# Kernel tuning notes

Measured on AMD Instinct MI355X. Metric: run time of the kernel, lower is better.

The kernel has to match this reference:

```python
import jax, jax.numpy as jnp
import numpy as np

B, Din, T, G = 8, 512, 1024, 128
DM, H, L, FF = 512, 8, 2, 2048
MAX_PERIOD = 10000.0


def _ln(x, s, b, eps=1e-5):
    m = x.mean(-1, keepdims=True)
    v = ((x - m) ** 2).mean(-1, keepdims=True)
    return (x - m) * jax.lax.rsqrt(v + eps) * s + b


def _rope(x, pos):
    # x: (B,H,S,Dh), pos: (S,)
    dh = x.shape[-1]
    half = dh // 2
    freqs = 1.0 / (MAX_PERIOD ** (jnp.arange(half, dtype=jnp.float32) / half))
    ang = pos[:, None] * freqs[None, :]              # (S, half)
    cos, sin = jnp.cos(ang), jnp.sin(ang)
    x1, x2 = x[..., :half], x[..., half:]
    return jnp.concatenate([x1 * cos - x2 * sin, x1 * sin + x2 * cos], axis=-1)


def _transformer(x, W_in, b_in, ln1_s, ln1_b, Wq, Wk, Wv, Wo, ls1,
                 ln2_s, ln2_b, W1, b1, W2, b2, ls2, lnf_s, lnf_b, W_out, b_out):
    # x: (B, Din, S) conv layout -> (B, S, DM)
    h = jnp.einsum('bds,de->bse', x, W_in) + b_in
    Bx, S, E = h.shape
    dh = E // H
    pos = jnp.arange(S, dtype=jnp.float32)
    scale = 1.0 / jnp.sqrt(jnp.asarray(dh, h.dtype))
    for l in range(Wq.shape[0]):
        y = _ln(h, ln1_s[l], ln1_b[l])
        q = (y @ Wq[l]).reshape(Bx, S, H, dh).transpose(0, 2, 1, 3)
        k = (y @ Wk[l]).reshape(Bx, S, H, dh).transpose(0, 2, 1, 3)
        v = (y @ Wv[l]).reshape(Bx, S, H, dh).transpose(0, 2, 1, 3)
        q, k = _rope(q, pos), _rope(k, pos)
        att = jax.nn.softmax(jnp.einsum('bhqd,bhkd->bhqk', q, k) * scale, axis=-1)
        o = jnp.einsum('bhqk,bhkd->bhqd', att, v).transpose(0, 2, 1, 3).reshape(Bx, S, E)
        h = h + ls1[l] * (o @ Wo[l])
        y = _ln(h, ln2_s[l], ln2_b[l])
        h = h + ls2[l] * (jax.nn.gelu(y @ W1[l] + b1[l]) @ W2[l] + b2[l])
    h = _ln(h, lnf_s, lnf_b)
    return (h @ W_out + b_out).transpose(0, 2, 1)  # (B, Din, S)


def _forward(features, alignment_matrix, num_segments_per_item, params):
    Bx, D, Tt = features.shape
    Gx = alignment_matrix.shape[1]
    ar_t = jnp.arange(Tt, dtype=jnp.int32)
    ar_g = jnp.arange(Gx, dtype=jnp.int32)
    group_mask = ar_g[None, :] < num_segments_per_item[:, None]          # (B,G)
    group_last = (alignment_matrix * ar_t.astype(features.dtype)).max(axis=2).astype(jnp.int32)  # (B,G)
    valid_last = jnp.where(group_mask, group_last, -1)
    frame_lengths = valid_last.max(axis=1) + 1                            # (B,)
    frame_mask = ar_t[None, :] < frame_lengths[:, None]                   # (B,T)
    last_for_count = jnp.where(group_mask, group_last, Tt + 1)
    num_q_before = jnp.sum(last_for_count[:, :, None] < ar_t[None, None, :], axis=1).astype(jnp.int32)  # (B,T)
    frame_dest = ar_t[None, :] + num_q_before                             # (B,T)
    query_dest = group_last + ar_g[None, :] + 1                           # (B,G)
    # mean-pooled query init
    summed = jnp.einsum('bgt,bdt->bgd', alignment_matrix, features)
    counts = jnp.maximum(alignment_matrix.sum(axis=2), 1.0)
    queries = (summed / counts[..., None]).transpose(0, 2, 1)             # (B,D,G)
    source_seq = jnp.concatenate([features, queries], axis=2)             # (B,D,T+G)
    dest = jnp.concatenate([frame_dest, query_dest], axis=1)              # (B,T+G)
    smask = jnp.concatenate([frame_mask, group_mask], axis=1)
    dest_m = jnp.where(smask, dest, Tt + Gx)
    perm = jnp.argsort(dest_m, axis=1)                                    # (B,T+G)
    interleaved = jnp.take_along_axis(source_seq, perm[:, None, :], axis=2)
    tout = _transformer(interleaved, *params)                             # (B,D,T+G)
    inv_perm = jnp.argsort(perm, axis=1)
    qpos = inv_perm[:, Tt:]                                               # (B,G)
    agg = jnp.take_along_axis(tout, qpos[:, None, :], axis=2)             # (B,D,G)
    return jnp.where(group_mask[:, None, :], agg, 0.0)


def setup_inputs() -> dict:
    key = jax.random.key(0)
    ks = jax.random.split(key, 8)
    rng = np.random.default_rng(0)
    align = np.zeros((B, G, T), np.float32)
    num_seg = np.zeros((B,), np.int32)
    for b in range(B):
        n = int(rng.integers(G // 2, G + 1))
        cuts = np.sort(rng.choice(np.arange(1, T), n - 1, replace=False))
        gid = np.searchsorted(cuts, np.arange(T), side='right')
        align[b, gid, np.arange(T)] = 1.0
        num_seg[b] = n
    s = 0.02
    return {
        'features': jax.random.normal(ks[0], (B, Din, T), jnp.float32),
        'alignment_matrix': jnp.asarray(align),
        'num_segments_per_item': jnp.asarray(num_seg),
        'W_in': jax.random.normal(ks[1], (Din, DM), jnp.float32) * s,
        'b_in': jnp.zeros((DM,), jnp.float32),
        'ln1_s': jnp.ones((L, DM), jnp.float32), 'ln1_b': jnp.zeros((L, DM), jnp.float32),
        'Wq': jax.random.normal(ks[2], (L, DM, DM), jnp.float32) * s,
        'Wk': jax.random.normal(ks[3], (L, DM, DM), jnp.float32) * s,
        'Wv': jax.random.normal(ks[4], (L, DM, DM), jnp.float32) * s,
        'Wo': jax.random.normal(ks[5], (L, DM, DM), jnp.float32) * s,
        'ls1': 0.01 * jnp.ones((L, DM), jnp.float32),
        'ln2_s': jnp.ones((L, DM), jnp.float32), 'ln2_b': jnp.zeros((L, DM), jnp.float32),
        'W1': jax.random.normal(ks[6], (L, DM, FF), jnp.float32) * s,
        'b1': jnp.zeros((L, FF), jnp.float32),
        'W2': jax.random.normal(ks[7], (L, FF, DM), jnp.float32) * s,
        'b2': jnp.zeros((L, DM), jnp.float32),
        'ls2': 0.01 * jnp.ones((L, DM), jnp.float32),
        'lnf_s': jnp.ones((DM,), jnp.float32), 'lnf_b': jnp.zeros((DM,), jnp.float32),
        'W_out': jax.random.normal(jax.random.fold_in(key, 9), (DM, Din), jnp.float32) * s,
        'b_out': jnp.zeros((Din,), jnp.float32),
    }


def reference(features, alignment_matrix, num_segments_per_item, W_in, b_in, ln1_s, ln1_b,
              Wq, Wk, Wv, Wo, ls1, ln2_s, ln2_b, W1, b1, W2, b2, ls2, lnf_s, lnf_b, W_out, b_out):
    params = (W_in, b_in, ln1_s, ln1_b, Wq, Wk, Wv, Wo, ls1,
              ln2_s, ln2_b, W1, b1, W2, b2, ls2, lnf_s, lnf_b, W_out, b_out)
    return _forward(features, alignment_matrix, num_segments_per_item, params)
```

## Files before the change

kernel.cpp:

```cpp
#include <hip/hip_runtime.h>
#include <hip/hip_bf16.h>
#include <math.h>

#define NB   8
#define NT   1024
#define NG   128
#define NS   1152
#define NDIN 512
#define NDM  512
#define NH   8
#define NDH  64
#define NFF  2048
#define NL   2

typedef __attribute__((ext_vector_type(4))) float  floatx4;
typedef __attribute__((ext_vector_type(8))) short  shortx8;

__device__ __forceinline__ float gelu_f(float x) {
    float u = 1.5957691216057308f * (x + 0.044715f * x * x * x);
    return x / (1.0f + __expf(-u));
}

__device__ __forceinline__ void gload_lds16(const void* g, void* l) {
    __builtin_amdgcn_global_load_lds((const __attribute__((address_space(1))) unsigned int*)g,
                                     (__attribute__((address_space(3))) unsigned int*)l, 16, 0, 0);
}

__device__ __forceinline__ short f2bfs(float x) {
    __hip_bfloat16 h = __float2bfloat16(x);
    return *(short*)&h;
}
__device__ __forceinline__ unsigned pack_bf2(float a, float b) {
    __hip_bfloat16 x = __float2bfloat16(a), y = __float2bfloat16(b);
    return ((unsigned)(*(unsigned short*)&y) << 16) | (*(unsigned short*)&x);
}

__global__ __launch_bounds__(256) void ropetab_k(float2* __restrict__ tab)
{
    const int idx = blockIdx.x * 256 + threadIdx.x;
    if (idx >= NS * 32) return;
    const int s = idx >> 5, i = idx & 31;
    const float fr = __expf(-(float)i * 0.28782313662425576f);
    const float ang = (float)s * fr;
    tab[idx] = make_float2(cosf(ang), sinf(ang));
}

__global__ __launch_bounds__(256) void pool_k(const float* __restrict__ align,
        const float* __restrict__ features, int* __restrict__ glast,
        float* __restrict__ queries)
{
    __shared__ float redf[256];
    __shared__ int   redi[256];
    __shared__ float aw[NT];
    const int bg = blockIdx.x;
    const int b = bg >> 7;
    const int tid = threadIdx.x;
    const float* arow = align + (size_t)bg * NT;
    float cnt = 0.f, last = 0.f;
    int tmin = NT;
    for (int t = tid; t < NT; t += 256) {
        float a = arow[t];
        cnt += a;
        last = fmaxf(last, a * (float)t);
        if (a > 0.f) tmin = min(tmin, t);
    }
    redf[tid] = cnt; __syncthreads();
    for (int s = 128; s > 0; s >>= 1) { if (tid < s) redf[tid] += redf[tid + s]; __syncthreads(); }
    float c = redf[0]; __syncthreads();
    redf[tid] = last; __syncthreads();
    for (int s = 128; s > 0; s >>= 1) { if (tid < s) redf[tid] = fmaxf(redf[tid], redf[tid + s]); __syncthreads(); }
    float l = redf[0];
    redi[tid] = tmin; __syncthreads();
    for (int s = 128; s > 0; s >>= 1) { if (tid < s) redi[tid] = min(redi[tid], redi[tid + s]); __syncthreads(); }
    const int t0 = redi[0];
    const int t1 = (int)l;
    if (tid == 0) glast[bg] = t1;
    __syncthreads();
    for (int t = t0 + tid; t <= t1; t += 256) aw[t - t0] = arow[t];
    __syncthreads();
    const float invc = 1.0f / fmaxf(c, 1.0f);
    for (int d = tid; d < NDIN; d += 256) {
        const float* frow = features + ((size_t)b * NDIN + d) * NT;
        float s = 0.f;
        for (int t = t0; t <= t1; ++t) s += aw[t - t0] * frow[t];
        queries[(size_t)bg * NDIN + d] = s * invc;
    }
}

__global__ __launch_bounds__(256) void rank_k(const int* __restrict__ glast,
        const int* __restrict__ nsegp, int* __restrict__ perm, int* __restrict__ qpos)
{
    __shared__ int dm[NS];
    __shared__ int gl[NG];
    const int b = blockIdx.y;
    const int tid = threadIdx.x;
    const int j = blockIdx.x * 256 + tid;
    if (tid < NG) gl[tid] = glast[b * NG + tid];
    const int ns = nsegp[b];
    __syncthreads();
    for (int jj = tid; jj < NS; jj += 256) {
        int d;
        if (jj < NT) {
            int t = jj, nq = 0, flen = 0;
            for (int g = 0; g < ns; ++g) {
                flen = max(flen, gl[g] + 1);
                nq += (gl[g] < t) ? 1 : 0;
            }
            d = (t < flen) ? (t + nq) : NS;
        } else {
            int g = jj - NT;
            d = (g < ns) ? (gl[g] + g + 1) : NS;
        }
        dm[jj] = d;
    }
    __syncthreads();
    if (j < NS) {
        const int my = dm[j];
        int r = 0;
        for (int t = 0; t < NS; ++t) {
            int v2 = dm[t];
            r += (v2 < my || (v2 == my && t < j)) ? 1 : 0;
        }
        perm[b * NS + r] = j;
        if (j >= NT) qpos[b * NG + (j - NT)] = r;
    }
}

__global__ __launch_bounds__(256) void buildx_k(const float* __restrict__ features,
        const float* __restrict__ queries, const int* __restrict__ perm,
        __hip_bfloat16* __restrict__ X)
{
    const int idx = blockIdx.x * 256 + threadIdx.x;
    if (idx >= NB * NS * NDIN) return;
    const int d = idx & (NDIN - 1);
    const int p = (idx >> 9) % NS;
    const int b = idx / (NS * NDIN);
    const int j = perm[b * NS + p];
    float v = (j < NT) ? features[((size_t)b * NDIN + d) * NT + j]
                       : queries[((size_t)(b * NG + (j - NT))) * NDIN + d];
    X[idx] = __float2bfloat16(v);
}

__device__ __forceinline__ void wtile(const float* __restrict__ src,
        __hip_bfloat16* __restrict__ dst, int K, int N, int i, int tid, short tile[32][33])
{
    const int gx = N / 32;
    const int n0 = (i % gx) * 32;
    const int k0 = (i / gx) * 32;
    {
        const int r = tid >> 3, c4 = (tid & 7) * 4;
        float4 v = *(const float4*)&src[(size_t)(k0 + r) * N + n0 + c4];
        tile[c4 + 0][r] = f2bfs(v.x);
        tile[c4 + 1][r] = f2bfs(v.y);
        tile[c4 + 2][r] = f2bfs(v.z);
        tile[c4 + 3][r] = f2bfs(v.w);
    }
    __syncthreads();
    {
        const int r = tid >> 3, c4 = (tid & 7) * 4;
        short* dp = (short*)dst + (size_t)(n0 + r) * K + k0 + c4;
        short4 v;
        v.x = tile[r][c4 + 0]; v.y = tile[r][c4 + 1];
        v.z = tile[r][c4 + 2]; v.w = tile[r][c4 + 3];
        *(short4*)dp = v;
    }
}

__global__ __launch_bounds__(256) void wtransall_k(
        const float* W_in, const float* Wq, const float* Wk, const float* Wv,
        const float* Wo, const float* W1, const float* W2, const float* W_out,
        __hip_bfloat16* w_inT, __hip_bfloat16* wqkvT0, __hip_bfloat16* wqkvT1,
        __hip_bfloat16* woT0, __hip_bfloat16* woT1,
        __hip_bfloat16* w1T0, __hip_bfloat16* w1T1,
        __hip_bfloat16* w2T0, __hip_bfloat16* w2T1, __hip_bfloat16* woutT)
{
    __shared__ short tile[32][33];
    const int tid = threadIdx.x;
    const int i = blockIdx.x;
    const float* src; __hip_bfloat16* dst; int K, N, ti;
    if (i < 256) { src = W_in; dst = w_inT; K = 512; N = 512; ti = i; }
    else if (i < 6400) {
        int r = i - 256;
        const int l = r / 3072; r -= l * 3072;
        const size_t o5 = (size_t)l * 262144, o2 = (size_t)l * 1048576;
        if (r < 256)       { src = Wq + o5; dst = (l ? wqkvT1 : wqkvT0);          K = 512;  N = 512;  ti = r; }
        else if (r < 512)  { src = Wk + o5; dst = (l ? wqkvT1 : wqkvT0) + 262144; K = 512;  N = 512;  ti = r - 256; }
        else if (r < 768)  { src = Wv + o5; dst = (l ? wqkvT1 : wqkvT0) + 524288; K = 512;  N = 512;  ti = r - 512; }
        else if (r < 1024) { src = Wo + o5; dst = (l ? woT1 : woT0);              K = 512;  N = 512;  ti = r - 768; }
        else if (r < 2048) { src = W1 + o2; dst = (l ? w1T1 : w1T0);              K = 512;  N = 2048; ti = r - 1024; }
        else               { src = W2 + o2; dst = (l ? w2T1 : w2T0);              K = 2048; N = 512;  ti = r - 2048; }
    }
    else { src = W_out; dst = woutT; K = 512; N = 512; ti = i - 6400; }
    wtile(src, dst, K, N, ti, tid, tile);
}

template <int EPI, int OUTBF>
__global__ __launch_bounds__(256) void bgemm_k(const __hip_bfloat16* __restrict__ A,
        const __hip_bfloat16* __restrict__ Bt, void* __restrict__ Cout,
        const float* __restrict__ bias, int M, int N, int K)
{
    __shared__ __align__(16) short As[128 * 32];
    __shared__ __align__(16) short Bs[128 * 32];
    const int tid = threadIdx.x;
    const int wave = tid >> 6, lane = tid & 63;
    const int quad = lane >> 4, l16 = lane & 15;
    const int wm = wave >> 1, wn = wave & 1;
    const size_t bm = (size_t)blockIdx.y * 128, bn = (size_t)blockIdx.x * 128;
    const int sw = (l16 >> 1) & 3;

    const short* Ag = (const short*)A;
    const short* Bg = (const short*)Bt;
    const int lrow = lane >> 2;
    const int lchunk = (lane & 3) ^ ((lane >> 3) & 3);

    floatx4 acc[4][4];
#pragma unroll
    for (int i = 0; i < 4; ++i)
#pragma unroll
        for (int j = 0; j < 4; ++j) acc[i][j] = (floatx4){0.f, 0.f, 0.f, 0.f};

    for (int k0 = 0; k0 < K; k0 += 32) {
        __syncthreads();
#pragma unroll
        for (int c = 0; c < 2; ++c) {
            const int r0 = (c * 4 + wave) * 16;
            const int row = r0 + lrow;
            gload_lds16(Ag + (bm + row) * (size_t)K + k0 + lchunk * 8, &As[r0 * 32]);
            gload_lds16(Bg + (bn + row) * (size_t)K + k0 + lchunk * 8, &Bs[r0 * 32]);
        }
        __syncthreads();
        shortx8 af[4], bf[4];
#pragma unroll
        for (int t = 0; t < 4; ++t) {
            af[t] = *(const shortx8*)&As[(wm * 64 + t * 16 + l16) * 32 + ((quad ^ sw) * 8)];
            bf[t] = *(const shortx8*)&Bs[(wn * 64 + t * 16 + l16) * 32 + ((quad ^ sw) * 8)];
        }
#pragma unroll
        for (int mt = 0; mt < 4; ++mt)
#pragma unroll
            for (int nt = 0; nt < 4; ++nt)
                acc[mt][nt] = __builtin_amdgcn_mfma_f32_16x16x32_bf16(af[mt], bf[nt], acc[mt][nt], 0, 0, 0);
    }
    const size_t mbase = bm + wm * 64;
    const size_t nbase = bn + wn * 64;
#pragma unroll
    for (int nt = 0; nt < 4; ++nt) {
        const size_t n = nbase + nt * 16 + l16;
        const float bz = bias ? bias[n] : 0.f;
#pragma unroll
        for (int mt = 0; mt < 4; ++mt) {
#pragma unroll
            for (int r = 0; r < 4; ++r) {
                const size_t m = mbase + mt * 16 + quad * 4 + r;
                const size_t off = m * N + n;
                float e = acc[mt][nt][r] + bz;
                if (EPI == 1) e = gelu_f(e);
                if (OUTBF) ((__hip_bfloat16*)Cout)[off] = __float2bfloat16(e);
                else       ((float*)Cout)[off] = e;
            }
        }
    }
}

__global__ __launch_bounds__(256) void bgemmqkv_k(const __hip_bfloat16* __restrict__ A,
        const __hip_bfloat16* __restrict__ Bt, __hip_bfloat16* __restrict__ qh,
        __hip_bfloat16* __restrict__ kh, __hip_bfloat16* __restrict__ vT,
        const float2* __restrict__ tab)
{
    __shared__ __align__(16) short As[128 * 32];
    __shared__ __align__(16) short Bs[128 * 32];
    const int tid = threadIdx.x;
    const int wave = tid >> 6, lane = tid & 63;
    const int quad = lane >> 4, l16 = lane & 15;
    const int wm = wave >> 1, wn = wave & 1;
    const size_t bm = (size_t)blockIdx.y * 128, bn = (size_t)blockIdx.x * 128;
    const int sw = (l16 >> 1) & 3;
    const int K = 512;

    const short* Ag = (const short*)A;
    const short* Bg = (const short*)Bt;
    const int lrow = lane >> 2;
    const int lchunk = (lane & 3) ^ ((lane >> 3) & 3);

    floatx4 acc[4][4];
#pragma unroll
    for (int i = 0; i < 4; ++i)
#pragma unroll
        for (int j = 0; j < 4; ++j) acc[i][j] = (floatx4){0.f, 0.f, 0.f, 0.f};

    for (int k0 = 0; k0 < K; k0 += 32) {
        __syncthreads();
#pragma unroll
        for (int c = 0; c < 2; ++c) {
            const int r0 = (c * 4 + wave) * 16;
            const int row = r0 + lrow;
            gload_lds16(Ag + (bm + row) * (size_t)K + k0 + lchunk * 8, &As[r0 * 32]);
            gload_lds16(Bg + (bn + row) * (size_t)K + k0 + lchunk * 8, &Bs[r0 * 32]);
        }
        __syncthreads();
        shortx8 af[4], bf[4];
#pragma unroll
        for (int t = 0; t < 4; ++t) {
            af[t] = *(const shortx8*)&As[(wm * 64 + t * 16 + l16) * 32 + ((quad ^ sw) * 8)];
            bf[t] = *(const shortx8*)&Bs[(wn * 64 + t * 16 + l16) * 32 + ((quad ^ sw) * 8)];
        }
#pragma unroll
        for (int mt = 0; mt < 4; ++mt)
#pragma unroll
            for (int nt = 0; nt < 4; ++nt)
                acc[mt][nt] = __builtin_amdgcn_mfma_f32_16x16x32_bf16(af[mt], bf[nt], acc[mt][nt], 0, 0, 0);
    }
    const int bidx = (int)(bm / NS);
    const int sbase = (int)(bm - (size_t)bidx * NS) + wm * 64;
    const int region = (int)(bn >> 9);
    if (region < 2) {
        const float qsc = region ? 1.0f : 0.18033688011112043f;
        short* dst = (short*)(region ? kh : qh);
        const int h = (int)((((int)bn & 511) + wn * 64) >> 6);
        const size_t hb = ((size_t)(bidx * NH + h)) * NS;
#pragma unroll
        for (int nt = 0; nt < 2; ++nt) {
            const int d = nt * 16 + l16;
            const float2* tp = tab + d;
#pragma unroll
            for (int mt = 0; mt < 4; ++mt) {
#pragma unroll
                for (int r = 0; r < 4; ++r) {
                    const int s = sbase + mt * 16 + quad * 4 + r;
                    float x1 = acc[mt][nt][r], x2 = acc[mt][nt + 2][r];
                    float2 cs = tp[s * 32];
                    short* dp = dst + (hb + s) * NDH + d;
                    dp[0]  = f2bfs(qsc * (x1 * cs.x - x2 * cs.y));
                    dp[32] = f2bfs(qsc * (x1 * cs.y + x2 * cs.x));
                }
            }
        }
    } else {
        const int base = (int)(bn - 1024) + wn * 64;
#pragma unroll
        for (int nt = 0; nt < 4; ++nt) {
            const int dfull = base + nt * 16 + l16;
            const int h = dfull >> 6, d = dfull & 63;
            short* vp = (short*)vT + ((size_t)(bidx * NH + h) * NDH + d) * NS;
#pragma unroll
            for (int mt = 0; mt < 4; ++mt)
#pragma unroll
                for (int r = 0; r < 4; ++r) {
                    const int s = sbase + mt * 16 + quad * 4 + r;
                    vp[s] = f2bfs(acc[mt][nt][r]);
                }
        }
    }
}

template <int EPI, int OUTBF>
__global__ __launch_bounds__(256) void bgemm64_k(const __hip_bfloat16* __restrict__ A,
        const __hip_bfloat16* __restrict__ Bt, void* __restrict__ Cout,
        const float* __restrict__ bias, const float* __restrict__ ls,
        const float* __restrict__ res, const int* __restrict__ nsegp, int M, int N, int K)
{
    __shared__ __align__(16) short As[64 * 32];
    __shared__ __align__(16) short Bs[128 * 32];
    const int tid = threadIdx.x;
    const int wave = tid >> 6, lane = tid & 63;
    const int quad = lane >> 4, l16 = lane & 15;
    const int wm = wave >> 1, wn = wave & 1;
    const size_t bm = (size_t)blockIdx.y * 64, bn = (size_t)blockIdx.x * 128;
    const int sw = (l16 >> 1) & 3;

    const short* Ag = (const short*)A;
    const short* Bg = (const short*)Bt;
    const int lrow = lane >> 2;
    const int lchunk = (lane & 3) ^ ((lane >> 3) & 3);

    floatx4 acc[2][4];
#pragma unroll
    for (int i = 0; i < 2; ++i)
#pragma unroll
        for (int j = 0; j < 4; ++j) acc[i][j] = (floatx4){0.f, 0.f, 0.f, 0.f};

    for (int k0 = 0; k0 < K; k0 += 32) {
        __syncthreads();
        {
            const int rA = wave * 16;
            gload_lds16(Ag + (bm + rA + lrow) * (size_t)K + k0 + lchunk * 8, &As[rA * 32]);
            const int rB = wave * 32;
            gload_lds16(Bg + (bn + rB + lrow) * (size_t)K + k0 + lchunk * 8, &Bs[rB * 32]);
            gload_lds16(Bg + (bn + rB + 16 + lrow) * (size_t)K + k0 + lchunk * 8, &Bs[(rB + 16) * 32]);
        }
        __syncthreads();
        shortx8 af[2], bf[4];
#pragma unroll
        for (int t = 0; t < 2; ++t)
            af[t] = *(const shortx8*)&As[(wm * 32 + t * 16 + l16) * 32 + ((quad ^ sw) * 8)];
#pragma unroll
        for (int t = 0; t < 4; ++t)
            bf[t] = *(const shortx8*)&Bs[(wn * 64 + t * 16 + l16) * 32 + ((quad ^ sw) * 8)];
#pragma unroll
        for (int mt = 0; mt < 2; ++mt)
#pragma unroll
            for (int nt = 0; nt < 4; ++nt)
                acc[mt][nt] = __builtin_amdgcn_mfma_f32_16x16x32_bf16(af[mt], bf[nt], acc[mt][nt], 0, 0, 0);
    }
    const size_t mbase = bm + wm * 32;
    const size_t nbase = bn + wn * 64;
#pragma unroll
    for (int nt = 0; nt < 4; ++nt) {
        const size_t n = nbase + nt * 16 + l16;
        const float bz = bias ? bias[n] : 0.f;
        const float lz = (EPI == 2) ? ls[n] : 0.f;
#pragma unroll
        for (int mt = 0; mt < 2; ++mt) {
#pragma unroll
            for (int r = 0; r < 4; ++r) {
                const size_t m = mbase + mt * 16 + quad * 4 + r;
                float e = acc[mt][nt][r] + bz;
                if (EPI == 4) {
                    const int b = (int)(m >> 7), g = (int)(m & 127);
                    float val = (g < nsegp[b]) ? e : 0.0f;
                    ((float*)Cout)[(size_t)b * (NDIN * NG) + n * NG + g] = val;
                } else {
                    const size_t off = m * N + n;
                    if (EPI == 2) e = res[off] + lz * e;
                    if (OUTBF) ((__hip_bfloat16*)Cout)[off] = __float2bfloat16(e);
                    else       ((float*)Cout)[off] = e;
                }
            }
        }
    }
}

__global__ __launch_bounds__(256) void lnw_k(const float* __restrict__ in,
        __hip_bfloat16* __restrict__ out, const float* __restrict__ gam, const float* __restrict__ bet)
{
    const int r = blockIdx.x * 4 + (threadIdx.x >> 6);
    const int t = threadIdx.x & 63;
    const float4* xp = (const float4*)(in + (size_t)r * NDM);
    float4 a = xp[t * 2], b4 = xp[t * 2 + 1];
    float s = a.x + a.y + a.z + a.w + b4.x + b4.y + b4.z + b4.w;
#pragma unroll
    for (int o = 1; o < 64; o <<= 1) s += __shfl_xor(s, o);
    const float mean = s * (1.0f / NDM);
    float dx[8] = {a.x - mean, a.y - mean, a.z - mean, a.w - mean,
                   b4.x - mean, b4.y - mean, b4.z - mean, b4.w - mean};
    float v = 0.f;
#pragma unroll
    for (int i = 0; i < 8; ++i) v += dx[i] * dx[i];
#pragma unroll
    for (int o = 1; o < 64; o <<= 1) v += __shfl_xor(v, o);
    const float inv = rsqrtf(v * (1.0f / NDM) + 1e-5f);
    const float4* gp = (const float4*)gam;
    const float4* bp = (const float4*)bet;
    float4 g0 = gp[t * 2], g1 = gp[t * 2 + 1], q0 = bp[t * 2], q1 = bp[t * 2 + 1];
    shortx8 o8;
    o8[0] = f2bfs(dx[0] * inv * g0.x + q0.x);
    o8[1] = f2bfs(dx[1] * inv * g0.y + q0.y);
    o8[2] = f2bfs(dx[2] * inv * g0.z + q0.z);
    o8[3] = f2bfs(dx[3] * inv * g0.w + q0.w);
    o8[4] = f2bfs(dx[4] * inv * g1.x + q1.x);
    o8[5] = f2bfs(dx[5] * inv * g1.y + q1.y);
    o8[6] = f2bfs(dx[6] * inv * g1.z + q1.z);
    o8[7] = f2bfs(dx[7] * inv * g1.w + q1.w);
    *(shortx8*)((short*)out + (size_t)r * NDM + t * 8) = o8;
}

__global__ __launch_bounds__(64) void lnwg_k(const float* __restrict__ h,
        __hip_bfloat16* __restrict__ out, const float* __restrict__ gam, const float* __restrict__ bet,
        const int* __restrict__ qpos)
{
    const int r = blockIdx.x, t = threadIdx.x;
    const int b = r >> 7;
    const int src = qpos[r];
    const float4* xp = (const float4*)(h + ((size_t)(b * NS + src)) * NDM);
    float4 a = xp[t * 2], b4 = xp[t * 2 + 1];
    float s = a.x + a.y + a.z + a.w + b4.x + b4.y + b4.z + b4.w;
#pragma unroll
    for (int o = 1; o < 64; o <<= 1) s += __shfl_xor(s, o);
    const float mean = s * (1.0f / NDM);
    float dx[8] = {a.x - mean, a.y - mean, a.z - mean, a.w - mean,
                   b4.x - mean, b4.y - mean, b4.z - mean, b4.w - mean};
    float v = 0.f;
#pragma unroll
    for (int i = 0; i < 8; ++i) v += dx[i] * dx[i];
#pragma unroll
    for (int o = 1; o < 64; o <<= 1) v += __shfl_xor(v, o);
    const float inv = rsqrtf(v * (1.0f / NDM) + 1e-5f);
    const float4* gp = (const float4*)gam;
    const float4* bp = (const float4*)bet;
    float4 g0 = gp[t * 2], g1 = gp[t * 2 + 1], q0 = bp[t * 2], q1 = bp[t * 2 + 1];
    shortx8 o8;
    o8[0] = f2bfs(dx[0] * inv * g0.x + q0.x);
    o8[1] = f2bfs(dx[1] * inv * g0.y + q0.y);
    o8[2] = f2bfs(dx[2] * inv * g0.z + q0.z);
    o8[3] = f2bfs(dx[3] * inv * g0.w + q0.w);
    o8[4] = f2bfs(dx[4] * inv * g1.x + q1.x);
    o8[5] = f2bfs(dx[5] * inv * g1.y + q1.y);
    o8[6] = f2bfs(dx[6] * inv * g1.z + q1.z);
    o8[7] = f2bfs(dx[7] * inv * g1.w + q1.w);
    *(shortx8*)((short*)out + (size_t)r * NDM + t * 8) = o8;
}

#define FKT 64
#define FKP 68
#define NTL (NS / FKT)
__global__ __launch_bounds__(256) void fattn_k(const __hip_bfloat16* __restrict__ qb,
        const __hip_bfloat16* __restrict__ kb, const __hip_bfloat16* __restrict__ vbT,
        __hip_bfloat16* __restrict__ o)
{
    __shared__ __align__(16) short Ks[FKT * FKP];
    __shared__ __align__(16) short Vt[NDH * FKP];
    __shared__ __align__(16) short Pl[64 * FKP];
    const int tid = threadIdx.x;
    const int wave = tid >> 6, lane = tid & 63;
    const int quad = lane >> 4, l16 = lane & 15;
    const int L = blockIdx.x;
    const int xcd = L & 7, sl = L >> 3;
    const int bh = (xcd << 3) | (sl & 7);
    const int q0 = (sl >> 3) * 64;
    const int bb = bh >> 3, hh = bh & 7;
    const short* qbase = (const short*)qb + (size_t)bh * NS * NDH;
    const short* kbase = (const short*)kb + (size_t)bh * NS * NDH;
    const short* vbase = (const short*)vbT + (size_t)bh * NDH * NS;

    shortx8 Qf0, Qf1;
    {
        const short* qp = qbase + (size_t)(q0 + wave * 16 + l16) * NDH + quad * 8;
        Qf0 = *(const shortx8*)qp;
        Qf1 = *(const shortx8*)(qp + 32);
    }
    floatx4 Oacc[4];
#pragma unroll
    for (int i = 0; i < 4; ++i) Oacc[i] = (floatx4){0.f, 0.f, 0.f, 0.f};
    float l_s = 0.f;

    const int sr = tid >> 2, sc = (tid & 3) * 16;
    const int prow = wave * 16 + l16;
    const short* kg = kbase + (size_t)sr * NDH + sc;
    const short* vg = vbase + (size_t)sr * NS + sc;
    shortx8 pk0 = *(const shortx8*)kg, pk1 = *(const shortx8*)(kg + 8);
    shortx8 pv0 = *(const shortx8*)vg, pv1 = *(const shortx8*)(vg + 8);

    for (int t = 0; t < NTL; ++t) {
        __syncthreads();
        *(shortx8*)&Ks[sr * FKP + sc]     = pk0;
        *(shortx8*)&Ks[sr * FKP + sc + 8] = pk1;
        *(shortx8*)&Vt[sr * FKP + sc]     = pv0;
        *(shortx8*)&Vt[sr * FKP + sc + 8] = pv1;
        __syncthreads();
        if (t + 1 < NTL) {
            kg += FKT * NDH; vg += FKT;
            pk0 = *(const shortx8*)kg; pk1 = *(const shortx8*)(kg + 8);
            pv0 = *(const shortx8*)vg; pv1 = *(const shortx8*)(vg + 8);
        }

        floatx4 S[4];
#pragma unroll
        for (int kbk = 0; kbk < 4; ++kbk) {
            shortx8 kf0 = *(const shortx8*)&Ks[(kbk * 16 + l16) * FKP + quad * 8];
            shortx8 kf1 = *(const shortx8*)&Ks[(kbk * 16 + l16) * FKP + 32 + quad * 8];
            floatx4 sa = (floatx4){0.f, 0.f, 0.f, 0.f};
            sa = __builtin_amdgcn_mfma_f32_16x16x32_bf16(kf0, Qf0, sa, 0, 0, 0);
            sa = __builtin_amdgcn_mfma_f32_16x16x32_bf16(kf1, Qf1, sa, 0, 0, 0);
            S[kbk] = sa;
        }
        float e[16];
        float rs = 0.f;
#pragma unroll
        for (int kbk = 0; kbk < 4; ++kbk)
#pragma unroll
            for (int i = 0; i < 4; ++i) {
                float ee = exp2f(S[kbk][i]);
                e[kbk * 4 + i] = ee;
                rs += ee;
            }
        rs += __shfl_xor(rs, 16);
        rs += __shfl_xor(rs, 32);
        l_s += rs;
#pragma unroll
        for (int kbk = 0; kbk < 4; ++kbk) {
            uint2 u;
            u.x = pack_bf2(e[kbk * 4 + 0], e[kbk * 4 + 1]);
            u.y = pack_bf2(e[kbk * 4 + 2], e[kbk * 4 + 3]);
            *(uint2*)&Pl[prow * FKP + kbk * 16 + quad * 4] = u;
        }
        __asm__ __volatile__("" ::: "memory");
        shortx8 Pf0 = *(const shortx8*)&Pl[prow * FKP + quad * 8];
        shortx8 Pf1 = *(const shortx8*)&Pl[prow * FKP + 32 + quad * 8];
#pragma unroll
        for (int ct = 0; ct < 4; ++ct) {
            shortx8 vf0 = *(const shortx8*)&Vt[(ct * 16 + l16) * FKP + quad * 8];
            shortx8 vf1 = *(const shortx8*)&Vt[(ct * 16 + l16) * FKP + 32 + quad * 8];
            Oacc[ct] = __builtin_amdgcn_mfma_f32_16x16x32_bf16(Pf0, vf0, Oacc[ct], 0, 0, 0);
            Oacc[ct] = __builtin_amdgcn_mfma_f32_16x16x32_bf16(Pf1, vf1, Oacc[ct], 0, 0, 0);
        }
    }
    float lr[4];
#pragma unroll
    for (int i = 0; i < 4; ++i) lr[i] = __shfl(l_s, quad * 4 + i);
#pragma unroll
    for (int i = 0; i < 4; ++i) {
        const float inv = 1.0f / lr[i];
        const int row = q0 + wave * 16 + quad * 4 + i;
        __hip_bfloat16* op = o + ((size_t)(bb * NS + row)) * NDM + hh * NDH + l16;
        op[0]  = __float2bfloat16(Oacc[0][i] * inv);
        op[16] = __float2bfloat16(Oacc[1][i] * inv);
        op[32] = __float2bfloat16(Oacc[2][i] * inv);
        op[48] = __float2bfloat16(Oacc[3][i] * inv);
    }
}

extern "C" void kernel_launch(void* const* d_in, const int* in_sizes, int n_in,
                              void* d_out, int out_size, void* d_ws, size_t ws_size,
                              hipStream_t stream) {
    const float* features = (const float*)d_in[0];
    const float* align    = (const float*)d_in[1];
    const int*   nseg     = (const int*)d_in[2];
    const float* W_in  = (const float*)d_in[3];
    const float* b_in  = (const float*)d_in[4];
    const float* ln1_s = (const float*)d_in[5];
    const float* ln1_b = (const float*)d_in[6];
    const float* Wq = (const float*)d_in[7];
    const float* Wk = (const float*)d_in[8];
    const float* Wv = (const float*)d_in[9];
    const float* Wo = (const float*)d_in[10];
    const float* ls1   = (const float*)d_in[11];
    const float* ln2_s = (const float*)d_in[12];
    const float* ln2_b = (const float*)d_in[13];
    const float* W1 = (const float*)d_in[14];
    const float* b1 = (const float*)d_in[15];
    const float* W2 = (const float*)d_in[16];
    const float* b2 = (const float*)d_in[17];
    const float* ls2   = (const float*)d_in[18];
    const float* lnf_s = (const float*)d_in[19];
    const float* lnf_b = (const float*)d_in[20];
    const float* W_out = (const float*)d_in[21];
    const float* b_out = (const float*)d_in[22];

    const size_t SZ_BSD = (size_t)NB * NS * NDM;

    float* p = (float*)d_ws;
    __hip_bfloat16* w_inT  = (__hip_bfloat16*)p;
    __hip_bfloat16* wqkvT0 = w_inT + 512 * 512;
    __hip_bfloat16* wqkvT1 = wqkvT0 + 1536 * 512;
    __hip_bfloat16* woT0   = wqkvT1 + 1536 * 512;
    __hip_bfloat16* woT1   = woT0 + 512 * 512;
    __hip_bfloat16* w1T0   = woT1 + 512 * 512;
    __hip_bfloat16* w1T1   = w1T0 + 2048 * 512;
    __hip_bfloat16* w2T0   = w1T1 + 2048 * 512;
    __hip_bfloat16* w2T1   = w2T0 + 512 * 2048;
    __hip_bfloat16* woutT  = w2T1 + 512 * 2048;
    int* glast = (int*)(woutT + 512 * 512);
    int* perm  = glast + NB * NG;
    int* qpos  = perm + NB * NS;
    float2* ropetab = (float2*)(qpos + NB * NG);
    p = (float*)(ropetab + NS * 32);

    float* hbuf = p; p += SZ_BSD;
    __hip_bfloat16* ybuf = (__hip_bfloat16*)p;  p += SZ_BSD / 2;
    __hip_bfloat16* obuf = (__hip_bfloat16*)p;  p += SZ_BSD / 2;
    __hip_bfloat16* ubuf = (__hip_bfloat16*)p;  p += SZ_BSD * 2;
    __hip_bfloat16* xin  = (__hip_bfloat16*)p;  p += SZ_BSD / 2;
    float* quer = p; p += (size_t)NB * NG * NDIN;
    __hip_bfloat16* hq = (__hip_bfloat16*)p; p += (size_t)NB * NG * NDM / 2;
    const size_t needed = (size_t)((char*)p - (char*)d_ws);
    if (ws_size < needed) return;

    __hip_bfloat16* qh = ubuf;
    __hip_bfloat16* kh = ubuf + SZ_BSD;
    __hip_bfloat16* vT = xin;

    ropetab_k<<<(NS * 32 + 255) / 256, 256, 0, stream>>>(ropetab);
    wtransall_k<<<6656, 256, 0, stream>>>(W_in, Wq, Wk, Wv, Wo, W1, W2, W_out,
            w_inT, wqkvT0, wqkvT1, woT0, woT1, w1T0, w1T1, w2T0, w2T1, woutT);
    pool_k<<<NB * NG, 256, 0, stream>>>(align, features, glast, quer);
    rank_k<<<dim3((NS + 255) / 256, NB), 256, 0, stream>>>(glast, nseg, perm, qpos);
    buildx_k<<<(NB * NS * NDIN + 255) / 256, 256, 0, stream>>>(features, quer, perm, xin);

    const int M = NB * NS;
    bgemm64_k<0, 0><<<dim3(NDM / 128, M / 64), 256, 0, stream>>>(xin, w_inT, hbuf, b_in, nullptr, nullptr, nullptr, M, NDM, NDIN);

    for (int l = 0; l < NL; ++l) {
        __hip_bfloat16* wqkvT = (l ? wqkvT1 : wqkvT0);
        __hip_bfloat16* woT   = (l ? woT1 : woT0);
        __hip_bfloat16* w1T   = (l ? w1T1 : w1T0);
        __hip_bfloat16* w2T   = (l ? w2T1 : w2T0);

        lnw_k<<<M / 4, 256, 0, stream>>>(hbuf, ybuf, ln1_s + l * NDM, ln1_b + l * NDM);
        bgemmqkv_k<<<dim3(1536 / 128, M / 128), 256, 0, stream>>>(ybuf, wqkvT, qh, kh, vT, ropetab);
        fattn_k<<<(NS / 64) * NH * NB, 256, 0, stream>>>(qh, kh, vT, obuf);
        bgemm64_k<2, 0><<<dim3(NDM / 128, M / 64), 256, 0, stream>>>(obuf, woT, hbuf, nullptr, ls1 + l * NDM, hbuf, nullptr, M, NDM, NDM);
        lnw_k<<<M / 4, 256, 0, stream>>>(hbuf, ybuf, ln2_s + l * NDM, ln2_b + l * NDM);
        bgemm_k<1, 1><<<dim3(NFF / 128, M / 128), 256, 0, stream>>>(ybuf, w1T, ubuf, b1 + l * NFF, M, NFF, NDM);
        bgemm64_k<2, 0><<<dim3(NDM / 128, M / 64), 256, 0, stream>>>(ubuf, w2T, hbuf, b2 + l * NDM, ls2 + l * NDM, hbuf, nullptr, M, NDM, NFF);
    }

    lnwg_k<<<NB * NG, 64, 0, stream>>>(hbuf, hq, lnf_s, lnf_b, qpos);
    bgemm64_k<4, 0><<<dim3(NDIN / 128, (NB * NG) / 64), 256, 0, stream>>>(hq, woutT, d_out, b_out, nullptr, nullptr, nseg, NB * NG, NDIN, NDM);
}
```

Baseline: 650.3 us.

## Double K-step per barrier in GEMMs and stage epilogues through LDS for vector stores

All three GEMM kernels now load a 64-wide K slab per barrier pair instead of 32, split across two LDS buffers. This halves the number of synchronisations per K loop and issues more loads in flight. The W1 and QKV GEMMs also write their epilogue results into swizzled LDS and then store them to global memory as 16-byte vectors, replacing scattered 2-byte stores; this includes the strided transposed V layout. The cost is twice the LDS per block, which may lower occupancy.

```diff
diff --git a/kernel.cpp b/kernel.cpp
--- a/kernel.cpp
+++ b/kernel.cpp
@@ -194,20 +194,19 @@
     wtile(src, dst, K, N, ti, tid, tile);
 }
 
-template <int EPI, int OUTBF>
-__global__ __launch_bounds__(256) void bgemm_k(const __hip_bfloat16* __restrict__ A,
-        const __hip_bfloat16* __restrict__ Bt, void* __restrict__ Cout,
+__global__ __launch_bounds__(256) void bgemmw1_k(const __hip_bfloat16* __restrict__ A,
+        const __hip_bfloat16* __restrict__ Bt, __hip_bfloat16* __restrict__ Cout,
         const float* __restrict__ bias, int M, int N, int K)
 {
-    __shared__ __align__(16) short As[128 * 32];
-    __shared__ __align__(16) short Bs[128 * 32];
+    __shared__ __align__(16) short SM[4][128 * 32];
+    short* As0 = SM[0]; short* As1 = SM[1];
+    short* Bs0 = SM[2]; short* Bs1 = SM[3];
     const int tid = threadIdx.x;
     const int wave = tid >> 6, lane = tid & 63;
     const int quad = lane >> 4, l16 = lane & 15;
     const int wm = wave >> 1, wn = wave & 1;
     const size_t bm = (size_t)blockIdx.y * 128, bn = (size_t)blockIdx.x * 128;
     const int sw = (l16 >> 1) & 3;
-
     const short* Ag = (const short*)A;
     const short* Bg = (const short*)Bt;
     const int lrow = lane >> 2;
@@ -219,46 +218,61 @@
 #pragma unroll
         for (int j = 0; j < 4; ++j) acc[i][j] = (floatx4){0.f, 0.f, 0.f, 0.f};
 
-    for (int k0 = 0; k0 < K; k0 += 32) {
+    for (int k0 = 0; k0 < K; k0 += 64) {
         __syncthreads();
 #pragma unroll
         for (int c = 0; c < 2; ++c) {
             const int r0 = (c * 4 + wave) * 16;
-            const int row = r0 + lrow;
-            gload_lds16(Ag + (bm + row) * (size_t)K + k0 + lchunk * 8, &As[r0 * 32]);
-            gload_lds16(Bg + (bn + row) * (size_t)K + k0 + lchunk * 8, &Bs[r0 * 32]);
+            const size_t ra = (bm + r0 + lrow) * (size_t)K + k0 + lchunk * 8;
+            const size_t rb = (bn + r0 + lrow) * (size_t)K + k0 + lchunk * 8;
+            gload_lds16(Ag + ra,      &As0[r0 * 32]);
+            gload_lds16(Ag + ra + 32, &As1[r0 * 32]);
+            gload_lds16(Bg + rb,      &Bs0[r0 * 32]);
+            gload_lds16(Bg + rb + 32, &Bs1[r0 * 32]);
         }
         __syncthreads();
-        shortx8 af[4], bf[4];
-#pragma unroll
-        for (int t = 0; t < 4; ++t) {
-            af[t] = *(const shortx8*)&As[(wm * 64 + t * 16 + l16) * 32 + ((quad ^ sw) * 8)];
-            bf[t] = *(const shortx8*)&Bs[(wn * 64 + t * 16 + l16) * 32 + ((quad ^ sw) * 8)];
-        }
-#pragma unroll
-        for (int mt = 0; mt < 4; ++mt)
-#pragma unroll
-            for (int nt = 0; nt < 4; ++nt)
-                acc[mt][nt] = __builtin_amdgcn_mfma_f32_16x16x32_bf16(af[mt], bf[nt], acc[mt][nt], 0, 0, 0);
-    }
+#pragma unroll
+        for (int h = 0; h < 2; ++h) {
+            const short* Asrc = h ? As1 : As0;
+            const short* Bsrc = h ? Bs1 : Bs0;
+            shortx8 af[4], bf[4];
+#pragma unroll
+            for (int t = 0; t < 4; ++t) {
+                af[t] = *(const shortx8*)&Asrc[(wm * 64 + t * 16 + l16) * 32 + ((quad ^ sw) * 8)];
+                bf[t] = *(const shortx8*)&Bsrc[(wn * 64 + t * 16 + l16) * 32 + ((quad ^ sw) * 8)];
+            }
+#pragma unroll
+            for (int mt = 0; mt < 4; ++mt)
+#pragma unroll
+                for (int nt = 0; nt < 4; ++nt)
+                    acc[mt][nt] = __builtin_amdgcn_mfma_f32_16x16x32_bf16(af[mt], bf[nt], acc[mt][nt], 0, 0, 0);
+        }
+    }
+    __syncthreads();
     const size_t mbase = bm + wm * 64;
     const size_t nbase = bn + wn * 64;
+    short* ep = &SM[wave][0];
 #pragma unroll
     for (int nt = 0; nt < 4; ++nt) {
         const size_t n = nbase + nt * 16 + l16;
-        const float bz = bias ? bias[n] : 0.f;
-#pragma unroll
-        for (int mt = 0; mt < 4; ++mt) {
+        const float bz = bias[n];
+        const int col = nt * 16 + l16;
+#pragma unroll
+        for (int mt = 0; mt < 4; ++mt)
 #pragma unroll
             for (int r = 0; r < 4; ++r) {
-                const size_t m = mbase + mt * 16 + quad * 4 + r;
-                const size_t off = m * N + n;
-                float e = acc[mt][nt][r] + bz;
-                if (EPI == 1) e = gelu_f(e);
-                if (OUTBF) ((__hip_bfloat16*)Cout)[off] = __float2bfloat16(e);
-                else       ((float*)Cout)[off] = e;
+                const int rl = mt * 16 + quad * 4 + r;
+                float e = gelu_f(acc[mt][nt][r] + bz);
+                ep[rl * 64 + (((col >> 3) ^ (rl & 7)) * 8) + (col & 7)] = f2bfs(e);
             }
-        }
+    }
+    __asm__ __volatile__("" ::: "memory");
+#pragma unroll
+    for (int c2 = 0; c2 < 8; ++c2) {
+        const int rl = c2 * 8 + (lane >> 3);
+        const int cc = lane & 7;
+        shortx8 v = *(const shortx8*)&ep[rl * 64 + ((cc ^ (rl & 7)) * 8)];
+        *(shortx8*)((short*)Cout + (mbase + rl) * N + nbase + cc * 8) = v;
     }
 }
 
@@ -267,8 +281,9 @@
         __hip_bfloat16* __restrict__ kh, __hip_bfloat16* __restrict__ vT,
         const float2* __restrict__ tab)
 {
-    __shared__ __align__(16) short As[128 * 32];
-    __shared__ __align__(16) short Bs[128 * 32];
+    __shared__ __align__(16) short SM[4][128 * 32];
+    short* As0 = SM[0]; short* As1 = SM[1];
+    short* Bs0 = SM[2]; short* Bs1 = SM[3];
     const int tid = threadIdx.x;
     const int wave = tid >> 6, lane = tid & 63;
     const int quad = lane >> 4, l16 = lane & 15;
@@ -276,7 +291,6 @@
     const size_t bm = (size_t)blockIdx.y * 128, bn = (size_t)blockIdx.x * 128;
     const int sw = (l16 >> 1) & 3;
     const int K = 512;
-
     const short* Ag = (const short*)A;
     const short* Bg = (const short*)Bt;
     const int lrow = lane >> 2;
@@ -288,86 +302,109 @@
 #pragma unroll
         for (int j = 0; j < 4; ++j) acc[i][j] = (floatx4){0.f, 0.f, 0.f, 0.f};
 
-    for (int k0 = 0; k0 < K; k0 += 32) {
+    for (int k0 = 0; k0 < K; k0 += 64) {
         __syncthreads();
 #pragma unroll
         for (int c = 0; c < 2; ++c) {
             const int r0 = (c * 4 + wave) * 16;
-            const int row = r0 + lrow;
-            gload_lds16(Ag + (bm + row) * (size_t)K + k0 + lchunk * 8, &As[r0 * 32]);
-            gload_lds16(Bg + (bn + row) * (size_t)K + k0 + lchunk * 8, &Bs[r0 * 32]);
+            const size_t ra = (bm + r0 + lrow) * (size_t)K + k0 + lchunk * 8;
+            const size_t rb = (bn + r0 + lrow) * (size_t)K + k0 + lchunk * 8;
+            gload_lds16(Ag + ra,      &As0[r0 * 32]);
+            gload_lds16(Ag + ra + 32, &As1[r0 * 32]);
+            gload_lds16(Bg + rb,      &Bs0[r0 * 32]);
+            gload_lds16(Bg + rb + 32, &Bs1[r0 * 32]);
         }
         __syncthreads();
-        shortx8 af[4], bf[4];
-#pragma unroll
-        for (int t = 0; t < 4; ++t) {
-            af[t] = *(const shortx8*)&As[(wm * 64 + t * 16 + l16) * 32 + ((quad ^ sw) * 8)];
-            bf[t] = *(const shortx8*)&Bs[(wn * 64 + t * 16 + l16) * 32 + ((quad ^ sw) * 8)];
-        }
-#pragma unroll
-        for (int mt = 0; mt < 4; ++mt)
-#pragma unroll
-            for (int nt = 0; nt < 4; ++nt)
-                acc[mt][nt] = __builtin_amdgcn_mfma_f32_16x16x32_bf16(af[mt], bf[nt], acc[mt][nt], 0, 0, 0);
-    }
+#pragma unroll
+        for (int h = 0; h < 2; ++h) {
+            const short* Asrc = h ? As1 : As0;
+            const short* Bsrc = h ? Bs1 : Bs0;
+            shortx8 af[4], bf[4];
+#pragma unroll
+            for (int t = 0; t < 4; ++t) {
+                af[t] = *(const shortx8*)&Asrc[(wm * 64 + t * 16 + l16) * 32 + ((quad ^ sw) * 8)];
+                bf[t] = *(const shortx8*)&Bsrc[(wn * 64 + t * 16 + l16) * 32 + ((quad ^ sw) * 8)];
+            }
+#pragma unroll
+            for (int mt = 0; mt < 4; ++mt)
+#pragma unroll
+                for (int nt = 0; nt < 4; ++nt)
+                    acc[mt][nt] = __builtin_amdgcn_mfma_f32_16x16x32_bf16(af[mt], bf[nt], acc[mt][nt], 0, 0, 0);
+        }
+    }
+    __syncthreads();
+    short* ep = &SM[wave][0];
     const int bidx = (int)(bm / NS);
     const int sbase = (int)(bm - (size_t)bidx * NS) + wm * 64;
     const int region = (int)(bn >> 9);
     if (region < 2) {
         const float qsc = region ? 1.0f : 0.18033688011112043f;
-        short* dst = (short*)(region ? kh : qh);
         const int h = (int)((((int)bn & 511) + wn * 64) >> 6);
-        const size_t hb = ((size_t)(bidx * NH + h)) * NS;
 #pragma unroll
         for (int nt = 0; nt < 2; ++nt) {
-            const int d = nt * 16 + l16;
-            const float2* tp = tab + d;
-#pragma unroll
-            for (int mt = 0; mt < 4; ++mt) {
+            const int d1 = nt * 16 + l16, d2 = d1 + 32;
+            const float2* tp = tab + d1;
+#pragma unroll
+            for (int mt = 0; mt < 4; ++mt)
 #pragma unroll
                 for (int r = 0; r < 4; ++r) {
-                    const int s = sbase + mt * 16 + quad * 4 + r;
+                    const int sl = mt * 16 + quad * 4 + r;
+                    const int s = sbase + sl;
                     float x1 = acc[mt][nt][r], x2 = acc[mt][nt + 2][r];
                     float2 cs = tp[s * 32];
-                    short* dp = dst + (hb + s) * NDH + d;
-                    dp[0]  = f2bfs(qsc * (x1 * cs.x - x2 * cs.y));
-                    dp[32] = f2bfs(qsc * (x1 * cs.y + x2 * cs.x));
+                    ep[sl * 64 + (((d1 >> 3) ^ (sl & 7)) * 8) + (d1 & 7)] = f2bfs(qsc * (x1 * cs.x - x2 * cs.y));
+                    ep[sl * 64 + (((d2 >> 3) ^ (sl & 7)) * 8) + (d2 & 7)] = f2bfs(qsc * (x1 * cs.y + x2 * cs.x));
                 }
-            }
+        }
+        __asm__ __volatile__("" ::: "memory");
+        short* dst = (short*)(region ? kh : qh) + ((size_t)(bidx * NH + h)) * NS * NDH;
+#pragma unroll
+        for (int c2 = 0; c2 < 8; ++c2) {
+            const int sl = c2 * 8 + (lane >> 3);
+            const int cc = lane & 7;
+            shortx8 v = *(const shortx8*)&ep[sl * 64 + ((cc ^ (sl & 7)) * 8)];
+            *(shortx8*)(dst + (size_t)(sbase + sl) * NDH + cc * 8) = v;
         }
     } else {
         const int base = (int)(bn - 1024) + wn * 64;
+        const int h = base >> 6;
 #pragma unroll
         for (int nt = 0; nt < 4; ++nt) {
-            const int dfull = base + nt * 16 + l16;
-            const int h = dfull >> 6, d = dfull & 63;
-            short* vp = (short*)vT + ((size_t)(bidx * NH + h) * NDH + d) * NS;
+            const int dl = nt * 16 + l16;
 #pragma unroll
             for (int mt = 0; mt < 4; ++mt)
 #pragma unroll
                 for (int r = 0; r < 4; ++r) {
-                    const int s = sbase + mt * 16 + quad * 4 + r;
-                    vp[s] = f2bfs(acc[mt][nt][r]);
+                    const int sl = mt * 16 + quad * 4 + r;
+                    ep[dl * 64 + (((sl >> 3) ^ (dl & 7)) * 8) + (sl & 7)] = f2bfs(acc[mt][nt][r]);
                 }
         }
-    }
-}
-
-template <int EPI, int OUTBF>
+        __asm__ __volatile__("" ::: "memory");
+        short* vp = (short*)vT + ((size_t)(bidx * NH + h)) * NDH * NS;
+#pragma unroll
+        for (int c2 = 0; c2 < 8; ++c2) {
+            const int dl = c2 * 8 + (lane >> 3);
+            const int cc = lane & 7;
+            shortx8 v = *(const shortx8*)&ep[dl * 64 + ((cc ^ (dl & 7)) * 8)];
+            *(shortx8*)(vp + (size_t)dl * NS + sbase + cc * 8) = v;
+        }
+    }
+}
+
+template <int EPI>
 __global__ __launch_bounds__(256) void bgemm64_k(const __hip_bfloat16* __restrict__ A,
         const __hip_bfloat16* __restrict__ Bt, void* __restrict__ Cout,
         const float* __restrict__ bias, const float* __restrict__ ls,
         const float* __restrict__ res, const int* __restrict__ nsegp, int M, int N, int K)
 {
-    __shared__ __align__(16) short As[64 * 32];
-    __shared__ __align__(16) short Bs[128 * 32];
+    __shared__ __align__(16) short As0[64 * 32], As1[64 * 32];
+    __shared__ __align__(16) short Bs0[128 * 32], Bs1[128 * 32];
     const int tid = threadIdx.x;
     const int wave = tid >> 6, lane = tid & 63;
     const int quad = lane >> 4, l16 = lane & 15;
     const int wm = wave >> 1, wn = wave & 1;
     const size_t bm = (size_t)blockIdx.y * 64, bn = (size_t)blockIdx.x * 128;
     const int sw = (l16 >> 1) & 3;
-
     const short* Ag = (const short*)A;
     const short* Bg = (const short*)Bt;
     const int lrow = lane >> 2;
@@ -379,28 +416,39 @@
 #pragma unroll
         for (int j = 0; j < 4; ++j) acc[i][j] = (floatx4){0.f, 0.f, 0.f, 0.f};
 
-    for (int k0 = 0; k0 < K; k0 += 32) {
+    for (int k0 = 0; k0 < K; k0 += 64) {
         __syncthreads();
         {
             const int rA = wave * 16;
-            gload_lds16(Ag + (bm + rA + lrow) * (size_t)K + k0 + lchunk * 8, &As[rA * 32]);
+            const size_t ra = (bm + rA + lrow) * (size_t)K + k0 + lchunk * 8;
+            gload_lds16(Ag + ra,      &As0[rA * 32]);
+            gload_lds16(Ag + ra + 32, &As1[rA * 32]);
             const int rB = wave * 32;
-            gload_lds16(Bg + (bn + rB + lrow) * (size_t)K + k0 + lchunk * 8, &Bs[rB * 32]);
-            gload_lds16(Bg + (bn + rB + 16 + lrow) * (size_t)K + k0 + lchunk * 8, &Bs[(rB + 16) * 32]);
+            const size_t rb0 = (bn + rB + lrow) * (size_t)K + k0 + lchunk * 8;
+            const size_t rb1 = (bn + rB + 16 + lrow) * (size_t)K + k0 + lchunk * 8;
+            gload_lds16(Bg + rb0,      &Bs0[rB * 32]);
+            gload_lds16(Bg + rb1,      &Bs0[(rB + 16) * 32]);
+            gload_lds16(Bg + rb0 + 32, &Bs1[rB * 32]);
+            gload_lds16(Bg + rb1 + 32, &Bs1[(rB + 16) * 32]);
         }
         __syncthreads();
-        shortx8 af[2], bf[4];
-#pragma unroll
-        for (int t = 0; t < 2; ++t)
-            af[t] = *(const shortx8*)&As[(wm * 32 + t * 16 + l16) * 32 + ((quad ^ sw) * 8)];
-#pragma unroll
-        for (int t = 0; t < 4; ++t)
-            bf[t] = *(const shortx8*)&Bs[(wn * 64 + t * 16 + l16) * 32 + ((quad ^ sw) * 8)];
-#pragma unroll
-        for (int mt = 0; mt < 2; ++mt)
-#pragma unroll
-            for (int nt = 0; nt < 4; ++nt)
-                acc[mt][nt] = __builtin_amdgcn_mfma_f32_16x16x32_bf16(af[mt], bf[nt], acc[mt][nt], 0, 0, 0);
+#pragma unroll
+        for (int h = 0; h < 2; ++h) {
+            const short* Asrc = h ? As1 : As0;
+            const short* Bsrc = h ? Bs1 : Bs0;
+            shortx8 af[2], bf[4];
+#pragma unroll
+            for (int t = 0; t < 2; ++t)
+                af[t] = *(const shortx8*)&Asrc[(wm * 32 + t * 16 + l16) * 32 + ((quad ^ sw) * 8)];
+#pragma unroll
+            for (int t = 0; t < 4; ++t)
+                bf[t] = *(const shortx8*)&Bsrc[(wn * 64 + t * 16 + l16) * 32 + ((quad ^ sw) * 8)];
+#pragma unroll
+            for (int mt = 0; mt < 2; ++mt)
+#pragma unroll
+                for (int nt = 0; nt < 4; ++nt)
+                    acc[mt][nt] = __builtin_amdgcn_mfma_f32_16x16x32_bf16(af[mt], bf[nt], acc[mt][nt], 0, 0, 0);
+        }
     }
     const size_t mbase = bm + wm * 32;
     const size_t nbase = bn + wn * 64;
@@ -422,8 +470,7 @@
                 } else {
                     const size_t off = m * N + n;
                     if (EPI == 2) e = res[off] + lz * e;
-                    if (OUTBF) ((__hip_bfloat16*)Cout)[off] = __float2bfloat16(e);
-                    else       ((float*)Cout)[off] = e;
+                    ((float*)Cout)[off] = e;
                 }
             }
         }
@@ -677,7 +724,7 @@
     buildx_k<<<(NB * NS * NDIN + 255) / 256, 256, 0, stream>>>(features, quer, perm, xin);
 
     const int M = NB * NS;
-    bgemm64_k<0, 0><<<dim3(NDM / 128, M / 64), 256, 0, stream>>>(xin, w_inT, hbuf, b_in, nullptr, nullptr, nullptr, M, NDM, NDIN);
+    bgemm64_k<0><<<dim3(NDM / 128, M / 64), 256, 0, stream>>>(xin, w_inT, hbuf, b_in, nullptr, nullptr, nullptr, M, NDM, NDIN);
 
     for (int l = 0; l < NL; ++l) {
         __hip_bfloat16* wqkvT = (l ? wqkvT1 : wqkvT0);
@@ -688,12 +735,12 @@
         lnw_k<<<M / 4, 256, 0, stream>>>(hbuf, ybuf, ln1_s + l * NDM, ln1_b + l * NDM);
         bgemmqkv_k<<<dim3(1536 / 128, M / 128), 256, 0, stream>>>(ybuf, wqkvT, qh, kh, vT, ropetab);
         fattn_k<<<(NS / 64) * NH * NB, 256, 0, stream>>>(qh, kh, vT, obuf);
-        bgemm64_k<2, 0><<<dim3(NDM / 128, M / 64), 256, 0, stream>>>(obuf, woT, hbuf, nullptr, ls1 + l * NDM, hbuf, nullptr, M, NDM, NDM);
+        bgemm64_k<2><<<dim3(NDM / 128, M / 64), 256, 0, stream>>>(obuf, woT, hbuf, nullptr, ls1 + l * NDM, hbuf, nullptr, M, NDM, NDM);
         lnw_k<<<M / 4, 256, 0, stream>>>(hbuf, ybuf, ln2_s + l * NDM, ln2_b + l * NDM);
-        bgemm_k<1, 1><<<dim3(NFF / 128, M / 128), 256, 0, stream>>>(ybuf, w1T, ubuf, b1 + l * NFF, M, NFF, NDM);
-        bgemm64_k<2, 0><<<dim3(NDM / 128, M / 64), 256, 0, stream>>>(ubuf, w2T, hbuf, b2 + l * NDM, ls2 + l * NDM, hbuf, nullptr, M, NDM, NFF);
+        bgemmw1_k<<<dim3(NFF / 128, M / 128), 256, 0, stream>>>(ybuf, w1T, ubuf, b1 + l * NFF, M, NFF, NDM);
+        bgemm64_k<2><<<dim3(NDM / 128, M / 64), 256, 0, stream>>>(ubuf, w2T, hbuf, b2 + l * NDM, ls2 + l * NDM, hbuf, nullptr, M, NDM, NFF);
     }
 
     lnwg_k<<<NB * NG, 64, 0, stream>>>(hbuf, hq, lnf_s, lnf_b, qpos);
-    bgemm64_k<4, 0><<<dim3(NDIN / 128, (NB * NG) / 64), 256, 0, stream>>>(hq, woutT, d_out, b_out, nullptr, nullptr, nseg, NB * NG, NDIN, NDM);
-}
+    bgemm64_k<4><<<dim3(NDIN / 128, (NB * NG) / 64), 256, 0, stream>>>(hq, woutT, d_out, b_out, nullptr, nullptr, nseg, NB * NG, NDIN, NDM);
+}
```

Result: faster. 635.4 us (-2.3%).
